# Performance work log

Hardware: AMD Instinct MI355X
Metric: run time of the kernel (lower is better)

The kernel has to match this reference:

```python
import jax, jax.numpy as jnp
import numpy as np

VOCAB, E, H = 50000, 128, 256
B, M, S, SQ = 64, 50, 20, 20
SEQEND = 2
HOPS = 3


def setup_inputs():
    key = jax.random.key(0)
    ks = jax.random.split(key, 24)
    story = jax.random.randint(ks[0], (B, M, S), 3, VOCAB, dtype=jnp.int32)
    story = story.at[:, :, -1].set(SEQEND)
    query = jax.random.randint(ks[1], (B, SQ), 3, VOCAB, dtype=jnp.int32)
    query = query.at[:, -1].set(SEQEND)

    def nrm(k, shape, scale=0.05):
        return jax.random.normal(k, shape, jnp.float32) * scale

    embed = nrm(ks[2], (VOCAB, E), 0.02).at[0].set(0.0)  # padding_idx=0 row zeroed
    return {
        "story": story, "query": query,
        "embed": embed,
        "w_ih": nrm(ks[3], (3 * H, E)), "w_hh": nrm(ks[4], (3 * H, H)),
        "b_ih": jnp.zeros((3 * H,), jnp.float32), "b_hh": jnp.zeros((3 * H,), jnp.float32),
        "w_m": nrm(ks[5], (H, H)),
        "ft_w1": nrm(ks[6], (H, H)), "ft_b1": jnp.zeros((H,), jnp.float32),
        "ft_w2": nrm(ks[7], (H, H)), "ft_b2": jnp.zeros((H,), jnp.float32),
        "g_w1": nrm(ks[8], (3 * H, 3 * H)), "g_b1": jnp.zeros((3 * H,), jnp.float32),
        "g_w2": nrm(ks[9], (3 * H, 3 * H)), "g_b2": jnp.zeros((3 * H,), jnp.float32),
        "f_w1": nrm(ks[10], (3 * H, 3 * H)), "f_b1": jnp.zeros((3 * H,), jnp.float32),
        "f_w2": nrm(ks[11], (H, 3 * H)), "f_b2": jnp.zeros((H,), jnp.float32),
        "v_w": nrm(ks[12], (VOCAB, H)),
    }


def _gru(x_tmaj, h0, w_ih, w_hh, b_ih, b_hh):
    """torch nn.GRU cell. x_tmaj: [T, N, E], h0: [N, H] -> outputs [T, N, H]."""
    def step(h, x):
        gi = x @ w_ih.T + b_ih
        gh = h @ w_hh.T + b_hh
        i_r, i_z, i_n = jnp.split(gi, 3, axis=-1)
        h_r, h_z, h_n = jnp.split(gh, 3, axis=-1)
        r = jax.nn.sigmoid(i_r + h_r)
        z = jax.nn.sigmoid(i_z + h_z)
        n = jnp.tanh(i_n + r * h_n)
        h2 = (1.0 - z) * n + z * h
        return h2, h2
    _, outs = jax.lax.scan(step, h0, x_tmaj)
    return outs


def reference(story, query, embed, w_ih, w_hh, b_ih, b_hh, w_m,
              ft_w1, ft_b1, ft_w2, ft_b2,
              g_w1, g_b1, g_w2, g_b2, f_w1, f_b1, f_w2, f_b2, v_w):
    Bd, Md, Sd = story.shape
    Hd = w_hh.shape[1]

    # --- story encoding. Original Python loop carries GRU hidden ACROSS batch
    # elements, so this is one GRU over the concatenated B*S time axis with M lanes.
    se = embed[story]                                          # [B,M,S,E]
    x = jnp.transpose(se, (0, 2, 1, 3)).reshape(Bd * Sd, Md, -1)  # [B*S, M, E]
    outs = _gru(x, jnp.zeros((Md, Hd), se.dtype), w_ih, w_hh, b_ih, b_hh)
    outs = jnp.transpose(outs.reshape(Bd, Sd, Md, Hd), (0, 2, 1, 3))  # [B,M,S,H]

    is_end = (story == SEQEND)
    idx = jnp.where(is_end.any(-1), jnp.argmax(is_end, axis=-1), Sd - 1)  # first <eos>, else last
    memory_slots = jnp.take_along_axis(outs, idx[:, :, None, None], axis=2)[:, :, 0, :]  # [B,M,H]

    # --- query encoding (fresh zero hidden, batched)
    qe = embed[query]                                          # [B,SQ,E]
    qouts = _gru(jnp.transpose(qe, (1, 0, 2)), jnp.zeros((Bd, Hd), qe.dtype),
                 w_ih, w_hh, b_ih, b_hh)
    qouts = jnp.transpose(qouts, (1, 0, 2))                    # [B,SQ,H]
    qis = (query == SEQEND)
    qidx = jnp.where(qis.any(-1), jnp.argmax(qis, axis=-1), query.shape[1] - 1)
    real_query = jnp.take_along_axis(qouts, qidx[:, None, None], axis=1)[:, 0, :]  # [B,H]

    # --- multi-hop attention over memory slots
    mem_key = memory_slots @ w_m.T                             # [B,M,H]
    scale = 1.0 / jnp.sqrt(jnp.asarray(Hd, memory_slots.dtype))
    o_k = real_query
    bufs = []
    for _ in range(HOPS):
        scores = jnp.einsum('bmh,bh->bm', mem_key, o_k) * scale
        attn = jax.nn.softmax(scores, axis=-1)
        buf = jnp.einsum('bm,bmh->bh', attn, memory_slots)
        bufs.append(buf)
        o_k = jax.nn.relu(buf @ ft_w1.T + ft_b1) @ ft_w2.T + ft_b2
    inp = jnp.stack(bufs, axis=1)                              # [B,3,H]

    # --- relation module over the 3 hop buffers (9 ordered pairs)
    n = HOPS
    left = jnp.tile(inp[:, None, :, :], (1, n, 1, 1)).reshape(Bd, n * n, Hd)   # [b,i*n+j]=inp[b,j]
    right = jnp.repeat(inp, n, axis=1)                                          # [b,i*n+j]=inp[b,i]
    qq = jnp.broadcast_to(real_query[:, None, :], (Bd, n * n, Hd))
    comb = jnp.concatenate([left, right, qq], axis=-1)          # [B,9,3H]
    g = jax.nn.relu(jax.nn.relu(comb @ g_w1.T + g_b1) @ g_w2.T + g_b2).sum(axis=1)
    reason = jax.nn.relu(g @ f_w1.T + f_b1) @ f_w2.T + f_b2     # [B,H]
    return reason @ v_w.T                                        # [B,VOCAB]
```

## Files before the change

### kernel.cpp

```cpp
#include <hip/hip_runtime.h>


typedef __attribute__((ext_vector_type(8))) short bf16x8;
typedef __attribute__((ext_vector_type(4))) float f32x4;
typedef __attribute__((ext_vector_type(4))) unsigned u32x4;

#define SPIN_MAX 16384

__device__ __forceinline__ unsigned short f2bf(float f) {
  union { float f; unsigned u; } v; v.f = f;
  unsigned x = v.u;
  return (unsigned short)((x + 0x7fffu + ((x >> 16) & 1u)) >> 16);
}

__global__ void zero_k(unsigned* p, int n) {
  int i = blockIdx.x * 256 + threadIdx.x;
  if (i < n) p[i] = 0u;
}

__global__ void idx_k(const int* __restrict__ story, const int* __restrict__ query,
                      int* __restrict__ idx_s, int* __restrict__ qidx) {
  int i = blockIdx.x * 256 + threadIdx.x;
  if (i < 3200) {
    const int* r = story + i * 20;
    int f = 19;
    for (int s = 19; s >= 0; --s) if (r[s] == 2) f = s;
    idx_s[i] = f;
  } else if (i < 3264) {
    int b = i - 3200;
    const int* r = query + b * 20;
    int f = 19;
    for (int s = 19; s >= 0; --s) if (r[s] == 2) f = s;
    qidx[b] = f;
  }
}

__global__ void gather_k(const int* __restrict__ story, const int* __restrict__ query,
                         const float* __restrict__ embed,
                         unsigned* __restrict__ Xs, unsigned* __restrict__ Xq) {
  long long id = (long long)blockIdx.x * 256 + threadIdx.x;
  if (id < 5242880LL) {
    int e2 = (int)(id & 63);
    int m  = (int)((id >> 6) & 63);
    int t  = (int)(id >> 12);
    unsigned val = 0u;
    if (m < 50) {
      int b = t / 20, s = t - b * 20;
      int tok = story[(b * 50 + m) * 20 + s];
      const float* e = embed + (size_t)tok * 128 + e2 * 2;
      val = (unsigned)f2bf(e[0]) | ((unsigned)f2bf(e[1]) << 16);
    }
    Xs[id] = val;
  } else {
    long long id2 = id - 5242880LL;
    int e2 = (int)(id2 & 63);
    int b  = (int)((id2 >> 6) & 63);
    int t  = (int)(id2 >> 12);
    int tok = query[b * 20 + t];
    const float* e = embed + (size_t)tok * 128 + e2 * 2;
    Xq[id2] = (unsigned)f2bf(e[0]) | ((unsigned)f2bf(e[1]) << 16);
  }
}

__device__ __forceinline__ void run_chain(
    const unsigned* __restrict__ X, int tokBase, int warm, int T,
    unsigned* __restrict__ hb, unsigned* __restrict__ flags,
    unsigned long long* __restrict__ s_h,
    const bf16x8 (&Bih)[3][4], const bf16x8 (&Bhh)[3][8],
    float br, float bz, float bin, float bhn,
    const int* __restrict__ eidx, float* __restrict__ outp,
    int chainIdx, bool isq,
    int lane, int wave, int lo, int quad, int col, int slice) {
  union U4 { u32x4 v4; bf16x8 v; };
  float h_own[4][4];
#pragma unroll
  for (int rt = 0; rt < 4; ++rt)
#pragma unroll
    for (int i = 0; i < 4; ++i) h_own[rt][i] = 0.f;

  for (int t = 0; t < T; ++t) {
    const unsigned* xt = X + (size_t)(tokBase + t) * 4096;
    f32x4 acc[4][3];
    f32x4 acchn[4];
#pragma unroll
    for (int rt = 0; rt < 4; ++rt) {
#pragma unroll
      for (int g = 0; g < 3; ++g) acc[rt][g] = (f32x4){0.f, 0.f, 0.f, 0.f};
      acchn[rt] = (f32x4){0.f, 0.f, 0.f, 0.f};
    }

    if (t > 0) {
      const unsigned* fl = flags + (size_t)(t - 1) * 16;
      for (int it = 0; it < SPIN_MAX; ++it) {
        unsigned v = 1u;
        if (lane < 16)
          v = __hip_atomic_load(fl + lane, __ATOMIC_RELAXED, __HIP_MEMORY_SCOPE_AGENT);
        if (__all(v != 0)) break;
      }
      asm volatile("" ::: "memory");
      const unsigned long long* hs =
          (const unsigned long long*)(hb + ((t - 1) & 1) * 8192);
      unsigned long long stg[16];
#pragma unroll
      for (int j = 0; j < 16; ++j)
        stg[j] = __hip_atomic_load(hs + wave * 1024 + j * 64 + lane,
                                   __ATOMIC_RELAXED, __HIP_MEMORY_SCOPE_AGENT);
#pragma unroll
      for (int rt = 0; rt < 4; ++rt) {
#pragma unroll
        for (int kt = 0; kt < 4; ++kt) {
          U4 ax;
          ax.v4 = *(const u32x4*)(xt + (rt * 16 + lo) * 64 + kt * 16 + quad * 4);
#pragma unroll
          for (int g = 0; g < 3; ++g)
            acc[rt][g] = __builtin_amdgcn_mfma_f32_16x16x32_bf16(
                ax.v, Bih[g][kt], acc[rt][g], 0, 0, 0);
        }
      }
#pragma unroll
      for (int j = 0; j < 16; ++j)
        s_h[wave * 1024 + j * 64 + lane] = stg[j];
      __syncthreads();
      const unsigned* sh32 = (const unsigned*)s_h;
#pragma unroll
      for (int kt = 0; kt < 8; ++kt) {
#pragma unroll
        for (int rt = 0; rt < 4; ++rt) {
          U4 ah;
          ah.v4 = *(const u32x4*)(sh32 + (rt * 16 + lo) * 128 + kt * 16 + quad * 4);
          acc[rt][0] = __builtin_amdgcn_mfma_f32_16x16x32_bf16(
              ah.v, Bhh[0][kt], acc[rt][0], 0, 0, 0);
          acc[rt][1] = __builtin_amdgcn_mfma_f32_16x16x32_bf16(
              ah.v, Bhh[1][kt], acc[rt][1], 0, 0, 0);
          acchn[rt] = __builtin_amdgcn_mfma_f32_16x16x32_bf16(
              ah.v, Bhh[2][kt], acchn[rt], 0, 0, 0);
        }
      }
    } else {
#pragma unroll
      for (int rt = 0; rt < 4; ++rt) {
#pragma unroll
        for (int kt = 0; kt < 4; ++kt) {
          U4 ax;
          ax.v4 = *(const u32x4*)(xt + (rt * 16 + lo) * 64 + kt * 16 + quad * 4);
#pragma unroll
          for (int g = 0; g < 3; ++g)
            acc[rt][g] = __builtin_amdgcn_mfma_f32_16x16x32_bf16(
                ax.v, Bih[g][kt], acc[rt][g], 0, 0, 0);
        }
      }
    }

    float h2v[4][4];
#pragma unroll
    for (int rt = 0; rt < 4; ++rt) {
#pragma unroll
      for (int i = 0; i < 4; ++i) {
        float r = 1.f / (1.f + __expf(-(acc[rt][0][i] + br)));
        float z = 1.f / (1.f + __expf(-(acc[rt][1][i] + bz)));
        float n = tanhf(acc[rt][2][i] + bin + r * (acchn[rt][i] + bhn));
        float h2 = (1.f - z) * n + z * h_own[rt][i];
        h_own[rt][i] = h2;
        h2v[rt][i] = h2;
      }
    }

    if (t + 1 < T) {
      unsigned* hd = hb + (t & 1) * 8192;
#pragma unroll
      for (int rt = 0; rt < 4; ++rt) {
#pragma unroll
        for (int i = 0; i < 4; ++i) {
          unsigned short mb = f2bf(h2v[rt][i]);
          int other = __shfl_xor((int)(unsigned)mb, 1);
          if ((lane & 1) == 0) {
            unsigned pack = (unsigned)mb | (((unsigned)other & 0xffffu) << 16);
            __hip_atomic_store(hd + (rt * 16 + quad * 4 + i) * 128 + (col >> 1), pack,
                               __ATOMIC_RELAXED, __HIP_MEMORY_SCOPE_AGENT);
          }
        }
      }
      asm volatile("s_waitcnt vmcnt(0)" ::: "memory");
      if (lane == 0)
        __hip_atomic_store(flags + (size_t)t * 16 + slice, 1u,
                           __ATOMIC_RELAXED, __HIP_MEMORY_SCOPE_AGENT);
    }

    if (!isq) {
      if (t >= warm) {
        int s = t - warm;
#pragma unroll
        for (int rt = 0; rt < 4; ++rt)
#pragma unroll
          for (int i = 0; i < 4; ++i) {
            int m = rt * 16 + quad * 4 + i;
            if (m < 50 && eidx[chainIdx * 50 + m] == s)
              outp[(size_t)(chainIdx * 50 + m) * 256 + col] = h2v[rt][i];
          }
      }
    } else {
#pragma unroll
      for (int rt = 0; rt < 4; ++rt)
#pragma unroll
        for (int i = 0; i < 4; ++i) {
          int m = rt * 16 + quad * 4 + i;
          if (eidx[m] == t)
            outp[(size_t)m * 256 + col] = h2v[rt][i];
        }
    }
  }
}

__global__ __launch_bounds__(256, 1) void gru_k(
    const float* __restrict__ w_ih, const float* __restrict__ w_hh,
    const float* __restrict__ b_ih, const float* __restrict__ b_hh,
    const unsigned* __restrict__ Xs, const unsigned* __restrict__ Xq,
    unsigned* hbs, unsigned* hbq,
    unsigned* flags_s, unsigned* flags_q,
    const int* __restrict__ idx_s, const int* __restrict__ qidx,
    float* __restrict__ mem_slots, float* __restrict__ real_q) {
  __shared__ unsigned long long s_h[4096];
  const int tid = threadIdx.x;
  const int c = blockIdx.x >> 2;
  const int wg4 = blockIdx.x & 3;
  const int lane = tid & 63;
  const int wave = tid >> 6;
  const int lo = lane & 15;
  const int quad = lane >> 4;
  const int slice = wg4 * 4 + wave;
  const int col = slice * 16 + lo;

  bf16x8 Bih[3][4], Bhh[3][8];
  for (int g = 0; g < 3; ++g) {
    const float* wr = w_ih + (size_t)(g * 256 + col) * 128;
    for (int kt = 0; kt < 4; ++kt) {
      const float* p = wr + kt * 32 + quad * 8;
      union { unsigned short us[8]; bf16x8 v; } u;
#pragma unroll
      for (int j = 0; j < 8; ++j) u.us[j] = f2bf(p[j]);
      Bih[g][kt] = u.v;
    }
    const float* wr2 = w_hh + (size_t)(g * 256 + col) * 256;
    for (int kt = 0; kt < 8; ++kt) {
      const float* p = wr2 + kt * 32 + quad * 8;
      union { unsigned short us[8]; bf16x8 v; } u;
#pragma unroll
      for (int j = 0; j < 8; ++j) u.us[j] = f2bf(p[j]);
      Bhh[g][kt] = u.v;
    }
  }
  const float br  = b_ih[col]       + b_hh[col];
  const float bz  = b_ih[256 + col] + b_hh[256 + col];
  const float bin = b_ih[512 + col];
  const float bhn = b_hh[512 + col];

  {
    int tokBase = (c == 0) ? 0 : (c - 1) * 20;
    int warm = (c == 0) ? 0 : 20;
    run_chain(Xs, tokBase, warm, warm + 20,
              hbs + (size_t)c * 16384, flags_s + (size_t)c * 640, s_h,
              Bih, Bhh, br, bz, bin, bhn, idx_s, mem_slots, c, false,
              lane, wave, lo, quad, col, slice);
  }
  if (c == 0) {
    __syncthreads();
    run_chain(Xq, 0, 0, 20, hbq, flags_q, s_h,
              Bih, Bhh, br, bz, bin, bhn, qidx, real_q, 0, true,
              lane, wave, lo, quad, col, slice);
  }
}

__global__ __launch_bounds__(256) void memkey_k(const float* __restrict__ slots,
                                                const float* __restrict__ w_m,
                                                float* __restrict__ mem_key) {
  __shared__ float A[4096];
  int tid = threadIdx.x;
  int r0 = blockIdx.x * 16;
  for (int i = tid; i < 4096; i += 256) A[i] = slots[(size_t)r0 * 256 + i];
  __syncthreads();
  float acc[16];
#pragma unroll
  for (int r = 0; r < 16; ++r) acc[r] = 0.f;
  const float* wr = w_m + (size_t)tid * 256;
  for (int k = 0; k < 256; ++k) {
    float wv = wr[k];
#pragma unroll
    for (int r = 0; r < 16; ++r) acc[r] += A[r * 256 + k] * wv;
  }
  for (int r = 0; r < 16; ++r) mem_key[(size_t)(r0 + r) * 256 + tid] = acc[r];
}

__global__ __launch_bounds__(256) void hops_k(const float* __restrict__ mem_key,
                                              const float* __restrict__ slots,
                                              const float* __restrict__ rq,
                                              const float* __restrict__ ft_w1,
                                              const float* __restrict__ ft_b1,
                                              const float* __restrict__ ft_w2,
                                              const float* __restrict__ ft_b2,
                                              float* __restrict__ bufs) {
  int b = blockIdx.x;
  int tid = threadIdx.x;
  int lane = tid & 63;
  int wv = tid >> 6;
  __shared__ float ok[256], attn[64], bufl[256], h1[256];
  ok[tid] = rq[(size_t)b * 256 + tid];
  __syncthreads();
  const float* key = mem_key + (size_t)b * 50 * 256;
  const float* slt = slots + (size_t)b * 50 * 256;
  for (int hop = 0; hop < 3; ++hop) {
    for (int m = wv; m < 50; m += 4) {
      const float* kr = key + m * 256;
      float p = kr[lane] * ok[lane] + kr[lane + 64] * ok[lane + 64] +
                kr[lane + 128] * ok[lane + 128] + kr[lane + 192] * ok[lane + 192];
      for (int off = 32; off; off >>= 1) p += __shfl_down(p, off);
      if (lane == 0) attn[m] = p * 0.0625f;
    }
    __syncthreads();
    if (tid == 0) {
      float mx = -1e30f;
      for (int m = 0; m < 50; ++m) mx = fmaxf(mx, attn[m]);
      float sm = 0.f;
      for (int m = 0; m < 50; ++m) { float e = __expf(attn[m] - mx); attn[m] = e; sm += e; }
      float inv = 1.f / sm;
      for (int m = 0; m < 50; ++m) attn[m] *= inv;
    }
    __syncthreads();
    float acc = 0.f;
    for (int m = 0; m < 50; ++m) acc += attn[m] * slt[m * 256 + tid];
    bufl[tid] = acc;
    bufs[(size_t)(b * 3 + hop) * 256 + tid] = acc;
    __syncthreads();
    float a1 = ft_b1[tid];
    const float* wr = ft_w1 + (size_t)tid * 256;
    for (int k = 0; k < 256; ++k) a1 += wr[k] * bufl[k];
    h1[tid] = fmaxf(a1, 0.f);
    __syncthreads();
    float a2 = ft_b2[tid];
    const float* w2r = ft_w2 + (size_t)tid * 256;
    for (int k = 0; k < 256; ++k) a2 += w2r[k] * h1[k];
    __syncthreads();
    ok[tid] = a2;
    __syncthreads();
  }
}

__global__ __launch_bounds__(256) void g1_k(const float* __restrict__ bufs,
                                            const float* __restrict__ rq,
                                            const float* __restrict__ w,
                                            const float* __restrict__ bias,
                                            float* __restrict__ out) {
  __shared__ float A[4 * 768];
  int tid = threadIdx.x;
  int r0 = blockIdx.x * 4;
  for (int i = tid; i < 4 * 768; i += 256) {
    int row = r0 + i / 768, k = i % 768;
    int bb = row / 9, p = row % 9;
    float v;
    if (k < 256)      v = bufs[(size_t)(bb * 3 + p % 3) * 256 + k];
    else if (k < 512) v = bufs[(size_t)(bb * 3 + p / 3) * 256 + (k - 256)];
    else              v = rq[(size_t)bb * 256 + (k - 512)];
    A[i] = v;
  }
  __syncthreads();
  for (int cc = 0; cc < 3; ++cc) {
    int c = cc * 256 + tid;
    float a0 = 0.f, a1 = 0.f, a2 = 0.f, a3 = 0.f;
    const float* wr = w + (size_t)c * 768;
    for (int k = 0; k < 768; ++k) {
      float wvl = wr[k];
      a0 += A[k] * wvl; a1 += A[768 + k] * wvl;
      a2 += A[1536 + k] * wvl; a3 += A[2304 + k] * wvl;
    }
    float bv = bias[c];
    out[(size_t)(r0 + 0) * 768 + c] = fmaxf(a0 + bv, 0.f);
    out[(size_t)(r0 + 1) * 768 + c] = fmaxf(a1 + bv, 0.f);
    out[(size_t)(r0 + 2) * 768 + c] = fmaxf(a2 + bv, 0.f);
    out[(size_t)(r0 + 3) * 768 + c] = fmaxf(a3 + bv, 0.f);
  }
}

__global__ __launch_bounds__(256) void g2_k(const float* __restrict__ t1,
                                            const float* __restrict__ w,
                                            const float* __restrict__ bias,
                                            float* __restrict__ out) {
  __shared__ float A[4 * 768];
  int tid = threadIdx.x;
  int r0 = blockIdx.x * 4;
  for (int i = tid; i < 4 * 768; i += 256) A[i] = t1[(size_t)r0 * 768 + i];
  __syncthreads();
  for (int cc = 0; cc < 3; ++cc) {
    int c = cc * 256 + tid;
    float a0 = 0.f, a1 = 0.f, a2 = 0.f, a3 = 0.f;
    const float* wr = w + (size_t)c * 768;
    for (int k = 0; k < 768; ++k) {
      float wvl = wr[k];
      a0 += A[k] * wvl; a1 += A[768 + k] * wvl;
      a2 += A[1536 + k] * wvl; a3 += A[2304 + k] * wvl;
    }
    float bv = bias[c];
    out[(size_t)(r0 + 0) * 768 + c] = fmaxf(a0 + bv, 0.f);
    out[(size_t)(r0 + 1) * 768 + c] = fmaxf(a1 + bv, 0.f);
    out[(size_t)(r0 + 2) * 768 + c] = fmaxf(a2 + bv, 0.f);
    out[(size_t)(r0 + 3) * 768 + c] = fmaxf(a3 + bv, 0.f);
  }
}

__global__ __launch_bounds__(256) void reason_k(const float* __restrict__ t2,
                                                const float* __restrict__ f_w1,
                                                const float* __restrict__ f_b1,
                                                const float* __restrict__ f_w2,
                                                const float* __restrict__ f_b2,
                                                float* __restrict__ reason) {
  int b = blockIdx.x;
  int tid = threadIdx.x;
  __shared__ float gs[768], h1[768];
  for (int j = tid; j < 768; j += 256) {
    float s = 0.f;
    for (int p = 0; p < 9; ++p) s += t2[(size_t)(b * 9 + p) * 768 + j];
    gs[j] = s;
  }
  __syncthreads();
  for (int jc = 0; jc < 3; ++jc) {
    int j = jc * 256 + tid;
    float a = f_b1[j];
    const float* wr = f_w1 + (size_t)j * 768;
    for (int k = 0; k < 768; ++k) a += wr[k] * gs[k];
    h1[j] = fmaxf(a, 0.f);
  }
  __syncthreads();
  {
    int j = tid;
    float a = f_b2[j];
    const float* wr = f_w2 + (size_t)j * 768;
    for (int k = 0; k < 768; ++k) a += wr[k] * h1[k];
    reason[(size_t)b * 256 + j] = a;
  }
}

__global__ __launch_bounds__(256) void vocab_k(const float* __restrict__ reason,
                                               const float* __restrict__ v_w,
                                               float* __restrict__ out) {
  __shared__ float A[32 * 256];
  int tid = threadIdx.x;
  int c = blockIdx.x * 256 + tid;
  for (int bc = 0; bc < 2; ++bc) {
    for (int i = tid; i < 32 * 256; i += 256) A[i] = reason[bc * 32 * 256 + i];
    __syncthreads();
    if (c < 50000) {
      float acc[32];
#pragma unroll
      for (int r = 0; r < 32; ++r) acc[r] = 0.f;
      const float* wr = v_w + (size_t)c * 256;
      for (int k = 0; k < 256; ++k) {
        float wvl = wr[k];
#pragma unroll
        for (int r = 0; r < 32; ++r) acc[r] += A[r * 256 + k] * wvl;
      }
      for (int r = 0; r < 32; ++r) out[(size_t)(bc * 32 + r) * 50000 + c] = acc[r];
    }
    __syncthreads();
  }
}

extern "C" void kernel_launch(void* const* d_in, const int* in_sizes, int n_in,
                              void* d_out, int out_size, void* d_ws, size_t ws_size,
                              hipStream_t stream) {
  (void)in_sizes; (void)n_in; (void)out_size; (void)ws_size;
  const int*   story = (const int*)d_in[0];
  const int*   query = (const int*)d_in[1];
  const float* embed = (const float*)d_in[2];
  const float* w_ih  = (const float*)d_in[3];
  const float* w_hh  = (const float*)d_in[4];
  const float* b_ih  = (const float*)d_in[5];
  const float* b_hh  = (const float*)d_in[6];
  const float* w_m   = (const float*)d_in[7];
  const float* ft_w1 = (const float*)d_in[8];
  const float* ft_b1 = (const float*)d_in[9];
  const float* ft_w2 = (const float*)d_in[10];
  const float* ft_b2 = (const float*)d_in[11];
  const float* g_w1  = (const float*)d_in[12];
  const float* g_b1  = (const float*)d_in[13];
  const float* g_w2  = (const float*)d_in[14];
  const float* g_b2  = (const float*)d_in[15];
  const float* f_w1  = (const float*)d_in[16];
  const float* f_b1  = (const float*)d_in[17];
  const float* f_w2  = (const float*)d_in[18];
  const float* f_b2  = (const float*)d_in[19];
  const float* v_w   = (const float*)d_in[20];
  float* out = (float*)d_out;

  char* ws = (char*)d_ws;
  unsigned* Xs      = (unsigned*)(ws + 0);
  unsigned* Xq      = (unsigned*)(ws + 20971520);
  unsigned* hbs     = (unsigned*)(ws + 21299200);
  unsigned* hbq     = (unsigned*)(ws + 25493504);
  unsigned* flags_s = (unsigned*)(ws + 25559040);
  unsigned* flags_q = (unsigned*)(ws + 25722880);
  int*      idx_s   = (int*)(ws + 25724160);
  int*      qidx    = (int*)(ws + 25736960);
  float*    mslots  = (float*)(ws + 25737216);
  float*    real_q  = (float*)(ws + 29014016);
  float*    mem_key = (float*)(ws + 0);
  float*    bufs    = (float*)(ws + 3276800);
  float*    t1      = (float*)(ws + 3473408);
  float*    t2      = (float*)(ws + 5242880);
  float*    reason  = (float*)(ws + 7012352);

  zero_k<<<162, 256, 0, stream>>>(flags_s, 41280);
  idx_k<<<13, 256, 0, stream>>>(story, query, idx_s, qidx);
  gather_k<<<20800, 256, 0, stream>>>(story, query, embed, Xs, Xq);
  gru_k<<<256, 256, 0, stream>>>(w_ih, w_hh, b_ih, b_hh, Xs, Xq, hbs, hbq,
                                 flags_s, flags_q, idx_s, qidx, mslots, real_q);
  memkey_k<<<200, 256, 0, stream>>>(mslots, w_m, mem_key);
  hops_k<<<64, 256, 0, stream>>>(mem_key, mslots, real_q,
                                 ft_w1, ft_b1, ft_w2, ft_b2, bufs);
  g1_k<<<144, 256, 0, stream>>>(bufs, real_q, g_w1, g_b1, t1);
  g2_k<<<144, 256, 0, stream>>>(t1, g_w2, g_b2, t2);
  reason_k<<<64, 256, 0, stream>>>(t2, f_w1, f_b1, f_w2, f_b2, reason);
  vocab_k<<<196, 256, 0, stream>>>(reason, v_w, out);
}
```

Before: 1.079 ms.

## Replace GRU step flags with per-word sequence tags and swizzle LDS hidden state

Drops the separate per-step flag array and its vmcnt wait plus flag store. Each packed bf16 hidden-state word is now written as a 64-bit value whose upper half carries the step number, so consumers poll the data itself until every tag matches. This removes one global round trip from the cross-workgroup critical path of the recurrence. It also adds an XOR swizzle to the LDS layout to cut bank conflicts on the MFMA operand reads, at the cost of doubling hidden-buffer traffic and zeroing a larger workspace region each call.

```diff
diff --git a/kernel.cpp b/kernel.cpp
--- a/kernel.cpp
+++ b/kernel.cpp
@@ -13,9 +13,9 @@
   return (unsigned short)((x + 0x7fffu + ((x >> 16) & 1u)) >> 16);
 }
 
-__global__ void zero_k(unsigned* p, int n) {
+__global__ void zero_k(u32x4* __restrict__ p, int n) {
   int i = blockIdx.x * 256 + threadIdx.x;
-  if (i < n) p[i] = 0u;
+  if (i < n) p[i] = (u32x4){0u, 0u, 0u, 0u};
 }
 
 __global__ void idx_k(const int* __restrict__ story, const int* __restrict__ query,
@@ -64,14 +64,15 @@
 
 __device__ __forceinline__ void run_chain(
     const unsigned* __restrict__ X, int tokBase, int warm, int T,
-    unsigned* __restrict__ hb, unsigned* __restrict__ flags,
+    unsigned long long* __restrict__ hb,
     unsigned long long* __restrict__ s_h,
     const bf16x8 (&Bih)[3][4], const bf16x8 (&Bhh)[3][8],
     float br, float bz, float bin, float bhn,
     const int* __restrict__ eidx, float* __restrict__ outp,
     int chainIdx, bool isq,
-    int lane, int wave, int lo, int quad, int col, int slice) {
+    int lane, int wave, int lo, int quad, int col) {
   union U4 { u32x4 v4; bf16x8 v; };
+  const int e = lo & 7;
   float h_own[4][4];
 #pragma unroll
   for (int rt = 0; rt < 4; ++rt)
@@ -90,21 +91,16 @@
     }
 
     if (t > 0) {
-      const unsigned* fl = flags + (size_t)(t - 1) * 16;
-      for (int it = 0; it < SPIN_MAX; ++it) {
-        unsigned v = 1u;
-        if (lane < 16)
-          v = __hip_atomic_load(fl + lane, __ATOMIC_RELAXED, __HIP_MEMORY_SCOPE_AGENT);
-        if (__all(v != 0)) break;
+      const unsigned long long* hs = hb + (size_t)((t - 1) & 1) * 8192;
+      const unsigned want = (unsigned)t;
+      unsigned long long stg0[16], stg1[16];
+#pragma unroll
+      for (int j = 0; j < 16; ++j) {
+        const unsigned long long* p = hs + (wave * 16 + j) * 128 + lane * 2;
+        stg0[j] = __hip_atomic_load(p,     __ATOMIC_RELAXED, __HIP_MEMORY_SCOPE_AGENT);
+        stg1[j] = __hip_atomic_load(p + 1, __ATOMIC_RELAXED, __HIP_MEMORY_SCOPE_AGENT);
       }
       asm volatile("" ::: "memory");
-      const unsigned long long* hs =
-          (const unsigned long long*)(hb + ((t - 1) & 1) * 8192);
-      unsigned long long stg[16];
-#pragma unroll
-      for (int j = 0; j < 16; ++j)
-        stg[j] = __hip_atomic_load(hs + wave * 1024 + j * 64 + lane,
-                                   __ATOMIC_RELAXED, __HIP_MEMORY_SCOPE_AGENT);
 #pragma unroll
       for (int rt = 0; rt < 4; ++rt) {
 #pragma unroll
@@ -117,9 +113,28 @@
                 ax.v, Bih[g][kt], acc[rt][g], 0, 0, 0);
         }
       }
-#pragma unroll
-      for (int j = 0; j < 16; ++j)
-        s_h[wave * 1024 + j * 64 + lane] = stg[j];
+      for (int it = 0; it < SPIN_MAX; ++it) {
+        bool ok = true;
+#pragma unroll
+        for (int j = 0; j < 16; ++j)
+          ok &= ((unsigned)(stg0[j] >> 32) == want) &
+                ((unsigned)(stg1[j] >> 32) == want);
+        if (__all(ok)) break;
+        __builtin_amdgcn_s_sleep(1);
+#pragma unroll
+        for (int j = 0; j < 16; ++j) {
+          const unsigned long long* p = hs + (wave * 16 + j) * 128 + lane * 2;
+          stg0[j] = __hip_atomic_load(p,     __ATOMIC_RELAXED, __HIP_MEMORY_SCOPE_AGENT);
+          stg1[j] = __hip_atomic_load(p + 1, __ATOMIC_RELAXED, __HIP_MEMORY_SCOPE_AGENT);
+        }
+      }
+#pragma unroll
+      for (int j = 0; j < 16; ++j) {
+        int row = wave * 16 + j;
+        unsigned long long v =
+            ((unsigned long long)(unsigned)stg1[j] << 32) | (unsigned)stg0[j];
+        s_h[row * 64 + (((lane >> 1) ^ (j & 7)) * 2 + (lane & 1))] = v;
+      }
       __syncthreads();
       const unsigned* sh32 = (const unsigned*)s_h;
 #pragma unroll
@@ -127,7 +142,8 @@
 #pragma unroll
         for (int rt = 0; rt < 4; ++rt) {
           U4 ah;
-          ah.v4 = *(const u32x4*)(sh32 + (rt * 16 + lo) * 128 + kt * 16 + quad * 4);
+          ah.v4 = *(const u32x4*)(sh32 + (rt * 16 + lo) * 128 +
+                                  (((kt * 4 + quad) ^ e) << 2));
           acc[rt][0] = __builtin_amdgcn_mfma_f32_16x16x32_bf16(
               ah.v, Bhh[0][kt], acc[rt][0], 0, 0, 0);
           acc[rt][1] = __builtin_amdgcn_mfma_f32_16x16x32_bf16(
@@ -166,7 +182,8 @@
     }
 
     if (t + 1 < T) {
-      unsigned* hd = hb + (t & 1) * 8192;
+      unsigned long long* hd = hb + (size_t)(t & 1) * 8192;
+      const unsigned long long tag = (unsigned long long)(unsigned)(t + 1) << 32;
 #pragma unroll
       for (int rt = 0; rt < 4; ++rt) {
 #pragma unroll
@@ -175,15 +192,12 @@
           int other = __shfl_xor((int)(unsigned)mb, 1);
           if ((lane & 1) == 0) {
             unsigned pack = (unsigned)mb | (((unsigned)other & 0xffffu) << 16);
-            __hip_atomic_store(hd + (rt * 16 + quad * 4 + i) * 128 + (col >> 1), pack,
+            __hip_atomic_store(hd + (rt * 16 + quad * 4 + i) * 128 + (col >> 1),
+                               tag | (unsigned long long)pack,
                                __ATOMIC_RELAXED, __HIP_MEMORY_SCOPE_AGENT);
           }
         }
       }
-      asm volatile("s_waitcnt vmcnt(0)" ::: "memory");
-      if (lane == 0)
-        __hip_atomic_store(flags + (size_t)t * 16 + slice, 1u,
-                           __ATOMIC_RELAXED, __HIP_MEMORY_SCOPE_AGENT);
     }
 
     if (!isq) {
@@ -215,19 +229,17 @@
     const float* __restrict__ w_ih, const float* __restrict__ w_hh,
     const float* __restrict__ b_ih, const float* __restrict__ b_hh,
     const unsigned* __restrict__ Xs, const unsigned* __restrict__ Xq,
-    unsigned* hbs, unsigned* hbq,
-    unsigned* flags_s, unsigned* flags_q,
+    unsigned long long* hbs, unsigned long long* hbq,
     const int* __restrict__ idx_s, const int* __restrict__ qidx,
     float* __restrict__ mem_slots, float* __restrict__ real_q) {
   __shared__ unsigned long long s_h[4096];
   const int tid = threadIdx.x;
   const int c = blockIdx.x >> 2;
-  const int wg4 = blockIdx.x & 3;
   const int lane = tid & 63;
   const int wave = tid >> 6;
   const int lo = lane & 15;
   const int quad = lane >> 4;
-  const int slice = wg4 * 4 + wave;
+  const int slice = (blockIdx.x & 3) * 4 + wave;
   const int col = slice * 16 + lo;
 
   bf16x8 Bih[3][4], Bhh[3][8];
@@ -258,15 +270,15 @@
     int tokBase = (c == 0) ? 0 : (c - 1) * 20;
     int warm = (c == 0) ? 0 : 20;
     run_chain(Xs, tokBase, warm, warm + 20,
-              hbs + (size_t)c * 16384, flags_s + (size_t)c * 640, s_h,
+              hbs + (size_t)c * 16384, s_h,
               Bih, Bhh, br, bz, bin, bhn, idx_s, mem_slots, c, false,
-              lane, wave, lo, quad, col, slice);
+              lane, wave, lo, quad, col);
   }
   if (c == 0) {
     __syncthreads();
-    run_chain(Xq, 0, 0, 20, hbq, flags_q, s_h,
+    run_chain(Xq, 0, 0, 20, hbq, s_h,
               Bih, Bhh, br, bz, bin, bhn, qidx, real_q, 0, true,
-              lane, wave, lo, quad, col, slice);
+              lane, wave, lo, quad, col);
   }
 }
 
@@ -490,27 +502,27 @@
   float* out = (float*)d_out;
 
   char* ws = (char*)d_ws;
-  unsigned* Xs      = (unsigned*)(ws + 0);
-  unsigned* Xq      = (unsigned*)(ws + 20971520);
-  unsigned* hbs     = (unsigned*)(ws + 21299200);
-  unsigned* hbq     = (unsigned*)(ws + 25493504);
-  unsigned* flags_s = (unsigned*)(ws + 25559040);
-  unsigned* flags_q = (unsigned*)(ws + 25722880);
-  int*      idx_s   = (int*)(ws + 25724160);
-  int*      qidx    = (int*)(ws + 25736960);
-  float*    mslots  = (float*)(ws + 25737216);
-  float*    real_q  = (float*)(ws + 29014016);
+  unsigned* Xs = (unsigned*)(ws + 0);
+  unsigned* Xq = (unsigned*)(ws + 20971520);
+  unsigned long long* hbs =
+      (unsigned long long*)(ws + 21299200);
+  unsigned long long* hbq =
+      (unsigned long long*)(ws + 29687808);
+  int*      idx_s   = (int*)(ws + 29818880);
+  int*      qidx    = (int*)(ws + 29831680);
+  float*    mslots  = (float*)(ws + 29831936);
+  float*    real_q  = (float*)(ws + 33108736);
   float*    mem_key = (float*)(ws + 0);
   float*    bufs    = (float*)(ws + 3276800);
   float*    t1      = (float*)(ws + 3473408);
   float*    t2      = (float*)(ws + 5242880);
   float*    reason  = (float*)(ws + 7012352);
 
-  zero_k<<<162, 256, 0, stream>>>(flags_s, 41280);
+  zero_k<<<2080, 256, 0, stream>>>((u32x4*)(ws + 21299200), 532480);
   idx_k<<<13, 256, 0, stream>>>(story, query, idx_s, qidx);
   gather_k<<<20800, 256, 0, stream>>>(story, query, embed, Xs, Xq);
   gru_k<<<256, 256, 0, stream>>>(w_ih, w_hh, b_ih, b_hh, Xs, Xq, hbs, hbq,
-                                 flags_s, flags_q, idx_s, qidx, mslots, real_q);
+                                 idx_s, qidx, mslots, real_q);
   memkey_k<<<200, 256, 0, stream>>>(mslots, w_m, mem_key);
   hops_k<<<64, 256, 0, stream>>>(mem_key, mslots, real_q,
                                  ft_w1, ft_b1, ft_w2, ft_b2, bufs);
```

Result: no change. 1.059 ms (-1.9%).
